# Performance work log

Measured on AMD Instinct MI355X. Metric: run time of the kernel, lower is better.

Reference implementation:

```python
import jax, jax.numpy as jnp
import numpy as np

_EPS = 1e-5

def _ln(x, g, b):
    m = jnp.mean(x, axis=-1, keepdims=True)
    v = jnp.var(x, axis=-1, keepdims=True)
    return (x - m) * jax.lax.rsqrt(v + _EPS) * g + b

def setup_inputs() -> dict:
    key = jax.random.key(0)
    ks = jax.random.split(key, 12)
    B, S, D = 8, 2048, 1024
    H = 2 * D          # hidden_dim = 2*n_embd
    A = H // 16        # adapt_dim = 128
    E = 8              # num_experts
    std = 1.0 / D ** 0.5
    astd = std * 0.01
    f = lambda k, shape, s: jax.random.normal(k, shape, dtype=jnp.float32) * s
    return {
        'x': f(ks[0], (B, S, D), 1.0),
        'expert_weights': f(ks[1], (B, S, E), 1.0),
        'w_up': f(ks[2], (H, D), std),
        'w_gate': f(ks[3], (H, D), std),
        'w_down': f(ks[4], (D, H), std),
        'w_pre': f(ks[5], (A, D), astd),
        'w_post': f(ks[6], (A, H), astd),
        'an_g': jnp.ones((A,), jnp.float32),
        'an_b': jnp.zeros((A,), jnp.float32),
        'w_aproj': f(ks[7], (H, A), astd),
        'w_exp': f(ks[8], (E, A, A), 0.01 / A ** 0.5),
        'eln_g': jnp.ones((E, A), jnp.float32),
        'eln_b': jnp.zeros((E, A), jnp.float32),
        'w_eproj': f(ks[9], (H, A), 0.01 / A ** 0.5),
        'w_out': f(ks[10], (D, H), 0.01 / A ** 0.5),
    }

def reference(x, expert_weights, w_up, w_gate, w_down, w_pre, w_post,
              an_g, an_b, w_aproj, w_exp, eln_g, eln_b, w_eproj, w_out):
    # ---- shared LLaDAExpert ----
    up = jnp.einsum('bsd,hd->bsh', x, w_up)
    gate = jnp.einsum('bsd,hd->bsh', x, w_gate)
    hidden = jax.nn.silu(gate) * up                      # [B,S,H]
    pre = jnp.einsum('bsd,ad->bsa', x, w_pre)            # pre_adapt(x), reused by experts
    adapt_in = _ln(pre, an_g, an_b)                      # [B,S,A]
    adapt_out = _ln(jnp.einsum('bsh,ah->bsa', hidden, w_post), an_g, an_b)
    aw = jax.nn.silu(jnp.clip(jnp.einsum('bsa,bta->bst', adapt_in, adapt_out), -5.0, 5.0))  # [B,S,S]
    adapt = jnp.einsum('bst,bta->bsa', aw, adapt_in)     # [B,S,A]
    hidden = hidden + 0.1 * jnp.einsum('bsa,ha->bsh', adapt, w_aproj)
    shared = jnp.einsum('bsh,dh->bsd', hidden, w_down)   # [B,S,D]
    combined = jnp.zeros_like(shared)
    E = w_exp.shape[0]
    for i in range(E):
        a = _ln(jnp.einsum('bsa,ca->bsc', pre, w_exp[i]), eln_g[i], eln_b[i])
        o = jnp.einsum('bsh,dh->bsd', jnp.einsum('bsc,hc->bsh', a, w_eproj), w_out)
        mask = expert_weights[:, :, i] > 0
        combined = jnp.where(mask[..., None], o, combined)
    return shared + 0.1 * combined
```

## Files before the change

### kernel.cpp

```cpp
#include <hip/hip_runtime.h>

#define TOK 16384
#define DD 1024
#define HH 2048
#define AA 128
#define EE 8
#define SS 2048
#define BB 8

typedef __attribute__((ext_vector_type(8))) short short8;
typedef __attribute__((ext_vector_type(4))) float floatx4;

__device__ __forceinline__ unsigned short f2b(float f) {
  unsigned u = __float_as_uint(f);
  u += 0x7fff + ((u >> 16) & 1);
  return (unsigned short)(u >> 16);
}
__device__ __forceinline__ float b2f(unsigned short h) {
  return __uint_as_float(((unsigned)h) << 16);
}

__device__ __forceinline__ void xcd_swizzle(int& bx, int& by) {
  const int nbx = gridDim.x, nby = gridDim.y;
  if ((nby & 7) == 0) {
    const int L = blockIdx.y * nbx + blockIdx.x;
    const int xcd = L & 7, idx = L >> 3;
    bx = idx % nbx;
    by = (xcd * (nby >> 3)) + idx / nbx;
  } else {
    bx = blockIdx.x; by = blockIdx.y;
  }
}

__device__ __forceinline__ void kloop_pipe(const short* Ap, int lda, const short* Bp, int ldb,
                                           short* As, short* Bs, int K,
                                           int tid, int q, int l15, int l7, int wm, int wn,
                                           floatx4 (*acc)[4])
{
  short8 pa[4], pb[4];
#pragma unroll
  for (int i = 0; i < 4; ++i) {
    pa[i] = *(const short8*)(Ap + (long)i*32*lda);
    pb[i] = *(const short8*)(Bp + (long)i*32*ldb);
  }
  for (int kt = 0; kt < K; kt += 64) {
#pragma unroll
    for (int i = 0; i < 4; ++i) {
      *(short8*)((char*)As + i*4096 + tid*16) = pa[i];
      *(short8*)((char*)Bs + i*4096 + tid*16) = pb[i];
    }
    __syncthreads();
    if (kt + 64 < K) {
#pragma unroll
      for (int i = 0; i < 4; ++i) {
        pa[i] = *(const short8*)(Ap + (long)i*32*lda + kt + 64);
        pb[i] = *(const short8*)(Bp + (long)i*32*ldb + kt + 64);
      }
    }
#pragma unroll
    for (int s = 0; s < 2; ++s) {
      short8 af[4], bf[4];
      const int slotoff = ((s*4 + q) ^ l7) * 16;
#pragma unroll
      for (int i = 0; i < 4; ++i) {
        af[i] = *(const short8*)((const char*)As + (wm*64 + i*16 + l15)*128 + slotoff);
        bf[i] = *(const short8*)((const char*)Bs + (wn*64 + i*16 + l15)*128 + slotoff);
      }
#pragma unroll
      for (int i = 0; i < 4; ++i)
#pragma unroll
        for (int j = 0; j < 4; ++j)
          acc[i][j] = __builtin_amdgcn_mfma_f32_16x16x32_bf16(af[i], bf[j], acc[i][j], 0, 0, 0);
    }
    __syncthreads();
  }
}

__global__ void cast_f32_bf16(const float* __restrict__ in, unsigned short* __restrict__ out, long n4) {
  long i = (long)blockIdx.x * blockDim.x + threadIdx.x;
  const long stride = (long)gridDim.x * blockDim.x;
  for (; i < n4; i += stride) {
    float4 v = ((const float4*)in)[i];
    ushort4 o;
    o.x = f2b(v.x); o.y = f2b(v.y); o.z = f2b(v.z); o.w = f2b(v.w);
    ((ushort4*)out)[i] = o;
  }
}

__global__ void transpose_cast(const float* __restrict__ in, unsigned short* __restrict__ out,
                               int R, int C) {
  __shared__ float t[32][33];
  const int lx = threadIdx.x & 31, ly = threadIdx.x >> 5;
  const int r0 = blockIdx.y * 32, c0 = blockIdx.x * 32;
#pragma unroll
  for (int i = 0; i < 32; i += 8)
    t[ly + i][lx] = in[(long)(r0 + ly + i) * C + (c0 + lx)];
  __syncthreads();
#pragma unroll
  for (int i = 0; i < 32; i += 8)
    out[(long)(c0 + ly + i) * R + (r0 + lx)] = f2b(t[lx][ly + i]);
}

template<int EPI>
__global__ __launch_bounds__(256)
void gemm_bt(const unsigned short* __restrict__ Ag, long sAz, int lda,
             const unsigned short* __restrict__ Bg, long sBz, int ldb,
             void* __restrict__ Cg, long sCz, int ldc,
             const unsigned short* __restrict__ Xg, long sXz, int ldx,
             int K)
{
  __shared__ __align__(16) short As[128*64];
  __shared__ __align__(16) short Bs[128*64];
  int bx, by; xcd_swizzle(bx, by);
  const int tid  = threadIdx.x;
  const int lane = tid & 63, wave = tid >> 6;
  const int q = lane >> 4, l15 = lane & 15, l7 = lane & 7;
  const int wm = wave & 1, wn = wave >> 1;

  const int arow = tid >> 3;
  const int kc8  = ((tid & 7) ^ (arow & 7)) * 8;

  const short* Ap = (const short*)Ag + (long)blockIdx.z*sAz + (long)(by*128 + arow)*lda + kc8;
  const short* Bp = (const short*)Bg + (long)blockIdx.z*sBz + (long)(bx*128 + arow)*ldb + kc8;

  floatx4 acc[4][4] = {};
  kloop_pipe(Ap, lda, Bp, ldb, As, Bs, K, tid, q, l15, l7, wm, wn, acc);

  const long cz = (long)blockIdx.z * sCz;
  const long xz = (long)blockIdx.z * sXz;
#pragma unroll
  for (int i = 0; i < 4; ++i)
#pragma unroll
    for (int j = 0; j < 4; ++j)
#pragma unroll
      for (int r = 0; r < 4; ++r) {
        const int row = by*128 + wm*64 + i*16 + q*4 + r;
        const int col = bx*128 + wn*64 + j*16 + l15;
        const long ci = cz + (long)row*ldc + col;
        float v = acc[i][j][r];
        if (EPI == 0) {
          ((float*)Cg)[ci] = v;
        } else if (EPI == 1) {
          v = v / (1.f + __expf(-v));
          ((unsigned short*)Cg)[ci] = f2b(v);
        } else if (EPI == 2) {
          float g = b2f(Xg[xz + (long)row*ldx + col]);
          ((unsigned short*)Cg)[ci] = f2b(v * g);
        } else if (EPI == 3) {
          ((unsigned short*)Cg)[ci] = f2b(v);
        } else if (EPI == 4) {
          v = fminf(fmaxf(v, -5.f), 5.f);
          v = v / (1.f + __expf(-v));
          ((unsigned short*)Cg)[ci] = f2b(v);
        } else if (EPI == 6) {
          ((unsigned short*)Cg)[ci] = f2b(0.1f * v);
        }
      }
}

__global__ __launch_bounds__(256)
void gemm_final(const unsigned short* __restrict__ hidp,
                const unsigned short* __restrict__ wdbp,
                const unsigned short* __restrict__ Fcp,
                const unsigned short* __restrict__ Wcp,
                float* __restrict__ outp)
{
  __shared__ __align__(16) short As[128*64];
  __shared__ __align__(16) short Bs[128*64];
  int bx, by; xcd_swizzle(bx, by);
  const int tid  = threadIdx.x;
  const int lane = tid & 63, wave = tid >> 6;
  const int q = lane >> 4, l15 = lane & 15, l7 = lane & 7;
  const int wm = wave & 1, wn = wave >> 1;
  const int arow = tid >> 3;
  const int kc8  = ((tid & 7) ^ (arow & 7)) * 8;

  floatx4 acc[4][4] = {};

  kloop_pipe((const short*)hidp + (long)(by*128 + arow)*HH + kc8, HH,
             (const short*)wdbp + (long)(bx*128 + arow)*HH + kc8, HH,
             As, Bs, HH, tid, q, l15, l7, wm, wn, acc);
  kloop_pipe((const short*)Fcp + (long)(by*128 + arow)*256 + kc8, 256,
             (const short*)Wcp + (long)(bx*128 + arow)*256 + kc8, 256,
             As, Bs, 256, tid, q, l15, l7, wm, wn, acc);

#pragma unroll
  for (int i = 0; i < 4; ++i)
#pragma unroll
    for (int j = 0; j < 4; ++j)
#pragma unroll
      for (int r = 0; r < 4; ++r) {
        const int row = by*128 + wm*64 + i*16 + q*4 + r;
        const int col = bx*128 + wn*64 + j*16 + l15;
        outp[(long)row*DD + col] = acc[i][j][r];
      }
}

__global__ void ln_rows(const float* __restrict__ X, const float* __restrict__ g,
                        const float* __restrict__ b, unsigned short* __restrict__ lnout,
                        unsigned short* __restrict__ rawout, unsigned short* __restrict__ tout)
{
  const int lane = threadIdx.x & 63, wave = threadIdx.x >> 6;
  const long t = (long)blockIdx.x*4 + wave;
  const float* x = X + t*AA;
  float x0 = x[lane], x1 = x[lane + 64];
  float s = x0 + x1, s2 = x0*x0 + x1*x1;
#pragma unroll
  for (int m = 1; m < 64; m <<= 1) {
    s  += __shfl_xor(s, m, 64);
    s2 += __shfl_xor(s2, m, 64);
  }
  float mean = s * (1.f/AA);
  float inv  = rsqrtf(s2*(1.f/AA) - mean*mean + 1e-5f);
  float y0 = (x0 - mean)*inv*g[lane] + b[lane];
  float y1 = (x1 - mean)*inv*g[lane+64] + b[lane+64];
  lnout[t*AA + lane]      = f2b(y0);
  lnout[t*AA + lane + 64] = f2b(y1);
  if (rawout) { rawout[t*AA+lane] = f2b(x0); rawout[t*AA+lane+64] = f2b(x1); }
  if (tout) {
    const long bb = t >> 11, si = t & (SS-1);
    tout[bb*(long)AA*SS + (long)lane*SS + si]      = f2b(y0);
    tout[bb*(long)AA*SS + (long)(lane+64)*SS + si] = f2b(y1);
  }
}

__global__ void expert_select_ln(const float* __restrict__ ew, const unsigned short* __restrict__ eall,
                                 const float* __restrict__ eg, const float* __restrict__ ebias,
                                 unsigned short* __restrict__ Fc)
{
  const int lane = threadIdx.x & 63, wave = threadIdx.x >> 6;
  const long t = (long)blockIdx.x*4 + wave;
  const float* w = ew + t*EE;
  int ie = -1;
#pragma unroll
  for (int i = 0; i < EE; ++i) if (w[i] > 0.f) ie = i;
  unsigned short o0 = 0, o1 = 0;
  if (ie >= 0) {
    float x0 = b2f(eall[t*(EE*AA) + ie*AA + lane]);
    float x1 = b2f(eall[t*(EE*AA) + ie*AA + lane + 64]);
    float s = x0 + x1, s2 = x0*x0 + x1*x1;
#pragma unroll
    for (int m = 1; m < 64; m <<= 1) { s += __shfl_xor(s, m, 64); s2 += __shfl_xor(s2, m, 64); }
    float mean = s * (1.f/AA);
    float inv  = rsqrtf(s2*(1.f/AA) - mean*mean + 1e-5f);
    o0 = f2b((x0-mean)*inv*eg[ie*AA+lane]    + ebias[ie*AA+lane]);
    o1 = f2b((x1-mean)*inv*eg[ie*AA+lane+64] + ebias[ie*AA+lane+64]);
  }
  Fc[t*256 + lane]      = o0;
  Fc[t*256 + lane + 64] = o1;
}

extern "C" void kernel_launch(void* const* d_in, const int* in_sizes, int n_in,
                              void* d_out, int out_size, void* d_ws, size_t ws_size,
                              hipStream_t stream)
{
  const float* x       = (const float*)d_in[0];
  const float* ew      = (const float*)d_in[1];
  const float* w_up    = (const float*)d_in[2];
  const float* w_gate  = (const float*)d_in[3];
  const float* w_down  = (const float*)d_in[4];
  const float* w_pre   = (const float*)d_in[5];
  const float* w_post  = (const float*)d_in[6];
  const float* an_g    = (const float*)d_in[7];
  const float* an_b    = (const float*)d_in[8];
  const float* w_aproj = (const float*)d_in[9];
  const float* w_exp   = (const float*)d_in[10];
  const float* eln_g   = (const float*)d_in[11];
  const float* eln_b   = (const float*)d_in[12];
  const float* w_eproj = (const float*)d_in[13];
  const float* w_out   = (const float*)d_in[14];

  char* ws = (char*)d_ws;
  size_t off = 0;
  auto take = [&](size_t bytes) { char* p = ws + off; off += (bytes + 255) & ~(size_t)255; return p; };

  unsigned short* Sc    = (unsigned short*)take((size_t)BB*SS*SS*2);
  unsigned short* xb    = Sc;
  unsigned short* eall  = (unsigned short*)((char*)Sc + (size_t)TOK*DD*2);
  unsigned short* hid   = (unsigned short*)take((size_t)TOK*HH*2);
  float*          pre   = (float*)take((size_t)TOK*AA*4);
  float*          postA = (float*)take((size_t)TOK*AA*4);
  unsigned short* Fc    = (unsigned short*)take((size_t)TOK*256*2);
  unsigned short* ain   = (unsigned short*)take((size_t)TOK*AA*2);
  unsigned short* ainT  = (unsigned short*)take((size_t)TOK*AA*2);
  unsigned short* aout  = (unsigned short*)take((size_t)TOK*AA*2);
  unsigned short* preb  = (unsigned short*)take((size_t)TOK*AA*2);
  unsigned short* wgb   = (unsigned short*)take((size_t)HH*DD*2);
  unsigned short* wub   = (unsigned short*)take((size_t)HH*DD*2);
  unsigned short* wdb   = (unsigned short*)take((size_t)DD*HH*2);
  unsigned short* wpostb= (unsigned short*)take((size_t)AA*HH*2);
  unsigned short* wpreb = (unsigned short*)take((size_t)AA*DD*2);
  unsigned short* wexpb = (unsigned short*)take((size_t)EE*AA*AA*2);
  unsigned short* Wc    = (unsigned short*)take((size_t)DD*256*2);
  (void)ws_size; (void)in_sizes; (void)n_in; (void)out_size;

  unsigned short* woutb  = hid;
  unsigned short* btT    = hid + (size_t)DD*HH;
  unsigned short* eprojT = btT;
  unsigned short* aprojT = btT + (size_t)AA*HH;

  cast_f32_bf16<<<1024, 256, 0, stream>>>(x,      xb,     (long)TOK*DD/4);
  cast_f32_bf16<<<256,  256, 0, stream>>>(w_gate, wgb,    (long)HH*DD/4);
  cast_f32_bf16<<<256,  256, 0, stream>>>(w_up,   wub,    (long)HH*DD/4);
  cast_f32_bf16<<<256,  256, 0, stream>>>(w_down, wdb,    (long)DD*HH/4);
  cast_f32_bf16<<<256,  256, 0, stream>>>(w_out,  woutb,  (long)DD*HH/4);
  cast_f32_bf16<<<64,   256, 0, stream>>>(w_post, wpostb, (long)AA*HH/4);
  cast_f32_bf16<<<32,   256, 0, stream>>>(w_pre,  wpreb,  (long)AA*DD/4);
  cast_f32_bf16<<<32,   256, 0, stream>>>(w_exp,  wexpb,  (long)EE*AA*AA/4);

  transpose_cast<<<dim3(AA/32, HH/32), 256, 0, stream>>>(w_eproj, eprojT, HH, AA);
  transpose_cast<<<dim3(AA/32, HH/32), 256, 0, stream>>>(w_aproj, aprojT, HH, AA);

  gemm_bt<6><<<dim3(1, DD/128, 2), 256, 0, stream>>>(
      woutb, (long)(wdb - woutb), HH,
      eprojT, (long)AA*HH, HH,
      Wc, AA, 256, nullptr, 0, 0, HH);

  gemm_bt<1><<<dim3(HH/128, TOK/128, 1), 256, 0, stream>>>(xb,0,DD, wgb,0,DD, hid,0,HH, nullptr,0,0, DD);
  gemm_bt<2><<<dim3(HH/128, TOK/128, 1), 256, 0, stream>>>(xb,0,DD, wub,0,DD, hid,0,HH, hid,0,HH, DD);

  gemm_bt<0><<<dim3(1, TOK/128, 1), 256, 0, stream>>>(xb,0,DD, wpreb,0,DD, pre,0,AA, nullptr,0,0, DD);
  ln_rows<<<TOK/4, 256, 0, stream>>>(pre, an_g, an_b, ain, preb, ainT);

  gemm_bt<3><<<dim3((EE*AA)/128, TOK/128, 1), 256, 0, stream>>>(preb,0,AA, wexpb,0,AA, eall,0,EE*AA, nullptr,0,0, AA);
  expert_select_ln<<<TOK/4, 256, 0, stream>>>(ew, eall, eln_g, eln_b, Fc);

  gemm_bt<0><<<dim3(1, TOK/128, 1), 256, 0, stream>>>(hid,0,HH, wpostb,0,HH, postA,0,AA, nullptr,0,0, HH);
  ln_rows<<<TOK/4, 256, 0, stream>>>(postA, an_g, an_b, aout, nullptr, nullptr);

  gemm_bt<4><<<dim3(SS/128, SS/128, BB), 256, 0, stream>>>(ain,(long)SS*AA,AA, aout,(long)SS*AA,AA,
                                                           Sc,(long)SS*SS,SS, nullptr,0,0, AA);
  gemm_bt<3><<<dim3(1, SS/128, BB), 256, 0, stream>>>(Sc,(long)SS*SS,SS, ainT,(long)AA*SS,SS,
                                                      Fc+AA,(long)SS*256,256, nullptr,0,0, SS);
  gemm_final<<<dim3(DD/128, TOK/128, 1), 256, 0, stream>>>(hid, wdb, Fc, Wc, (float*)d_out);
}
```

Measured before the change: 602.8 us.

## Add 256x256 tiled GEMM with direct-to-LDS loads for big GEMMs

```diff
diff --git a/kernel.cpp b/kernel.cpp
--- a/kernel.cpp
+++ b/kernel.cpp
@@ -30,6 +30,188 @@
   } else {
     bx = blockIdx.x; by = blockIdx.y;
   }
+}
+
+
+__device__ __forceinline__ void gload16(const short* g, short* l) {
+  __builtin_amdgcn_global_load_lds((__attribute__((address_space(1))) void*)(void*)g,
+                                   (__attribute__((address_space(3))) void*)l, 16, 0, 0);
+}
+
+__device__ __forceinline__ void stage_tile(const short* src, int ld, short* dst, int wave) {
+#pragma unroll
+  for (int i = 0; i < 4; ++i)
+    gload16(src + (long)i*64*ld, dst + i*4096 + wave*512);
+}
+
+__device__ __forceinline__ void ktile256(const char* Ab, const char* Bb,
+                                         short* Ad, short* Bd,
+                                         const short* nA, int nlda,
+                                         const short* nB, int nldb,
+                                         bool st, int wave,
+                                         int aOff, int bOff, int slot0, int slot1,
+                                         floatx4 (*acc)[4])
+{
+  short8 af[4][2], bf[4][2];
+#pragma unroll
+  for (int m = 0; m < 4; ++m) {
+    af[m][0] = *(const short8*)(Ab + aOff + m*2048 + slot0);
+    af[m][1] = *(const short8*)(Ab + aOff + m*2048 + slot1);
+  }
+#pragma unroll
+  for (int n = 0; n < 2; ++n) {
+    bf[n][0] = *(const short8*)(Bb + bOff + n*2048 + slot0);
+    bf[n][1] = *(const short8*)(Bb + bOff + n*2048 + slot1);
+  }
+  __builtin_amdgcn_s_barrier();
+  asm volatile("s_waitcnt lgkmcnt(0)" ::: "memory");
+  __builtin_amdgcn_s_setprio(1);
+#pragma unroll
+  for (int m = 0; m < 4; ++m)
+#pragma unroll
+    for (int n = 0; n < 2; ++n) {
+      acc[m][n] = __builtin_amdgcn_mfma_f32_16x16x32_bf16(af[m][0], bf[n][0], acc[m][n], 0, 0, 0);
+      acc[m][n] = __builtin_amdgcn_mfma_f32_16x16x32_bf16(af[m][1], bf[n][1], acc[m][n], 0, 0, 0);
+    }
+  __builtin_amdgcn_s_setprio(0);
+  __builtin_amdgcn_s_barrier();
+#pragma unroll
+  for (int n = 2; n < 4; ++n) {
+    bf[n][0] = *(const short8*)(Bb + bOff + n*2048 + slot0);
+    bf[n][1] = *(const short8*)(Bb + bOff + n*2048 + slot1);
+  }
+  __builtin_amdgcn_s_barrier();
+  asm volatile("s_waitcnt lgkmcnt(0)" ::: "memory");
+  __builtin_amdgcn_s_setprio(1);
+#pragma unroll
+  for (int m = 0; m < 4; ++m)
+#pragma unroll
+    for (int n = 2; n < 4; ++n) {
+      acc[m][n] = __builtin_amdgcn_mfma_f32_16x16x32_bf16(af[m][0], bf[n][0], acc[m][n], 0, 0, 0);
+      acc[m][n] = __builtin_amdgcn_mfma_f32_16x16x32_bf16(af[m][1], bf[n][1], acc[m][n], 0, 0, 0);
+    }
+  __builtin_amdgcn_s_setprio(0);
+  __builtin_amdgcn_s_barrier();
+#pragma unroll
+  for (int m = 0; m < 4; ++m) {
+    af[m][0] = *(const short8*)(Ab + aOff + (m+4)*2048 + slot0);
+    af[m][1] = *(const short8*)(Ab + aOff + (m+4)*2048 + slot1);
+  }
+  if (st) stage_tile(nB, nldb, Bd, wave);
+  __builtin_amdgcn_s_barrier();
+  asm volatile("s_waitcnt lgkmcnt(0)" ::: "memory");
+  __builtin_amdgcn_s_setprio(1);
+#pragma unroll
+  for (int m = 0; m < 4; ++m)
+#pragma unroll
+    for (int n = 0; n < 2; ++n) {
+      acc[m+4][n] = __builtin_amdgcn_mfma_f32_16x16x32_bf16(af[m][0], bf[n][0], acc[m+4][n], 0, 0, 0);
+      acc[m+4][n] = __builtin_amdgcn_mfma_f32_16x16x32_bf16(af[m][1], bf[n][1], acc[m+4][n], 0, 0, 0);
+    }
+  __builtin_amdgcn_s_setprio(0);
+  __builtin_amdgcn_s_barrier();
+  if (st) stage_tile(nA, nlda, Ad, wave);
+  __builtin_amdgcn_s_barrier();
+  __builtin_amdgcn_s_setprio(1);
+#pragma unroll
+  for (int m = 0; m < 4; ++m)
+#pragma unroll
+    for (int n = 2; n < 4; ++n) {
+      acc[m+4][n] = __builtin_amdgcn_mfma_f32_16x16x32_bf16(af[m][0], bf[n][0], acc[m+4][n], 0, 0, 0);
+      acc[m+4][n] = __builtin_amdgcn_mfma_f32_16x16x32_bf16(af[m][1], bf[n][1], acc[m+4][n], 0, 0, 0);
+    }
+  __builtin_amdgcn_s_setprio(0);
+  if (st) asm volatile("s_waitcnt vmcnt(8)" ::: "memory");
+  else    asm volatile("s_waitcnt vmcnt(0)" ::: "memory");
+  __builtin_amdgcn_s_barrier();
+}
+
+template<int EPI>
+__global__ __launch_bounds__(512, 2)
+void gemm256(const unsigned short* __restrict__ Ag, int lda,
+             const unsigned short* __restrict__ Bg, int ldb,
+             void* __restrict__ Cg, int ldc,
+             const unsigned short* __restrict__ Xg, int ldx,
+             int K1,
+             const unsigned short* __restrict__ A2g, int lda2,
+             const unsigned short* __restrict__ B2g, int ldb2,
+             int K2)
+{
+  __shared__ __align__(16) short As[2][256*64];
+  __shared__ __align__(16) short Bs[2][256*64];
+  int bx, by; xcd_swizzle(bx, by);
+  const int tid = threadIdx.x;
+  const int lane = tid & 63, wave = tid >> 6;
+  const int q = lane >> 4, l15 = lane & 15;
+  const int wm = wave >> 2, wn = wave & 3;
+
+  const int arow = tid >> 3;
+  const int kc8  = ((tid & 7) ^ (arow & 7)) * 8;
+
+  const short* a1 = (const short*)Ag + (long)(by*256 + arow)*lda + kc8;
+  const short* b1 = (const short*)Bg + (long)(bx*256 + arow)*ldb + kc8;
+  const short* a2 = A2g ? (const short*)A2g + (long)(by*256 + arow)*lda2 + kc8 : (const short*)0;
+  const short* b2 = B2g ? (const short*)B2g + (long)(bx*256 + arow)*ldb2 + kc8 : (const short*)0;
+  const int nt1 = K1 >> 6, nt = (K1 + K2) >> 6, niter = nt >> 1;
+
+  auto tA = [&](int T, const short*& p, int& ld) {
+    if (T < nt1) { p = a1 + T*64; ld = lda; } else { p = a2 + (T - nt1)*64; ld = lda2; }
+  };
+  auto tB = [&](int T, const short*& p, int& ld) {
+    if (T < nt1) { p = b1 + T*64; ld = ldb; } else { p = b2 + (T - nt1)*64; ld = ldb2; }
+  };
+
+  const int aOff  = (wm*128 + l15) * 128;
+  const int bOff  = (wn*64  + l15) * 128;
+  const int l7    = l15 & 7;
+  const int slot0 = ((0*4 + q) ^ l7) * 16;
+  const int slot1 = ((1*4 + q) ^ l7) * 16;
+
+  floatx4 acc[8][4] = {};
+
+  stage_tile(a1, lda, As[0], wave);
+  stage_tile(b1, ldb, Bs[0], wave);
+  {
+    const short *pa, *pb; int la, lb;
+    tA(1, pa, la); tB(1, pb, lb);
+    stage_tile(pa, la, As[1], wave);
+    stage_tile(pb, lb, Bs[1], wave);
+  }
+  asm volatile("s_waitcnt vmcnt(8)" ::: "memory");
+  __builtin_amdgcn_s_barrier();
+
+  for (int i = 0; i < niter; ++i) {
+    const int t2 = 2*i + 2;
+    const bool st = t2 < nt;
+    const short *na = a1, *nb = b1; int nla = lda, nlb = ldb;
+    if (st) { tA(t2, na, nla); tB(t2, nb, nlb); }
+    ktile256((const char*)As[0], (const char*)Bs[0], As[0], Bs[0],
+             na, nla, nb, nlb, st, wave, aOff, bOff, slot0, slot1, acc);
+    if (st) { tA(t2+1, na, nla); tB(t2+1, nb, nlb); }
+    ktile256((const char*)As[1], (const char*)Bs[1], As[1], Bs[1],
+             na, nla, nb, nlb, st, wave, aOff, bOff, slot0, slot1, acc);
+  }
+
+#pragma unroll
+  for (int m = 0; m < 8; ++m)
+#pragma unroll
+    for (int n = 0; n < 4; ++n)
+#pragma unroll
+      for (int r = 0; r < 4; ++r) {
+        const int row = by*256 + wm*128 + m*16 + q*4 + r;
+        const int col = bx*256 + wn*64  + n*16 + l15;
+        const long ci = (long)row*ldc + col;
+        float v = acc[m][n][r];
+        if (EPI == 0) {
+          ((float*)Cg)[ci] = v;
+        } else if (EPI == 1) {
+          v = v / (1.f + __expf(-v));
+          ((unsigned short*)Cg)[ci] = f2b(v);
+        } else if (EPI == 2) {
+          float g = b2f(Xg[(long)row*ldx + col]);
+          ((unsigned short*)Cg)[ci] = f2b(v * g);
+        }
+      }
 }
 
 __device__ __forceinline__ void kloop_pipe(const short* Ap, int lda, const short* Bp, int ldb,
@@ -158,44 +340,6 @@
       }
 }
 
-__global__ __launch_bounds__(256)
-void gemm_final(const unsigned short* __restrict__ hidp,
-                const unsigned short* __restrict__ wdbp,
-                const unsigned short* __restrict__ Fcp,
-                const unsigned short* __restrict__ Wcp,
-                float* __restrict__ outp)
-{
-  __shared__ __align__(16) short As[128*64];
-  __shared__ __align__(16) short Bs[128*64];
-  int bx, by; xcd_swizzle(bx, by);
-  const int tid  = threadIdx.x;
-  const int lane = tid & 63, wave = tid >> 6;
-  const int q = lane >> 4, l15 = lane & 15, l7 = lane & 7;
-  const int wm = wave & 1, wn = wave >> 1;
-  const int arow = tid >> 3;
-  const int kc8  = ((tid & 7) ^ (arow & 7)) * 8;
-
-  floatx4 acc[4][4] = {};
-
-  kloop_pipe((const short*)hidp + (long)(by*128 + arow)*HH + kc8, HH,
-             (const short*)wdbp + (long)(bx*128 + arow)*HH + kc8, HH,
-             As, Bs, HH, tid, q, l15, l7, wm, wn, acc);
-  kloop_pipe((const short*)Fcp + (long)(by*128 + arow)*256 + kc8, 256,
-             (const short*)Wcp + (long)(bx*128 + arow)*256 + kc8, 256,
-             As, Bs, 256, tid, q, l15, l7, wm, wn, acc);
-
-#pragma unroll
-  for (int i = 0; i < 4; ++i)
-#pragma unroll
-    for (int j = 0; j < 4; ++j)
-#pragma unroll
-      for (int r = 0; r < 4; ++r) {
-        const int row = by*128 + wm*64 + i*16 + q*4 + r;
-        const int col = bx*128 + wn*64 + j*16 + l15;
-        outp[(long)row*DD + col] = acc[i][j][r];
-      }
-}
-
 __global__ void ln_rows(const float* __restrict__ X, const float* __restrict__ g,
                         const float* __restrict__ b, unsigned short* __restrict__ lnout,
                         unsigned short* __restrict__ rawout, unsigned short* __restrict__ tout)
@@ -316,8 +460,10 @@
       eprojT, (long)AA*HH, HH,
       Wc, AA, 256, nullptr, 0, 0, HH);
 
-  gemm_bt<1><<<dim3(HH/128, TOK/128, 1), 256, 0, stream>>>(xb,0,DD, wgb,0,DD, hid,0,HH, nullptr,0,0, DD);
-  gemm_bt<2><<<dim3(HH/128, TOK/128, 1), 256, 0, stream>>>(xb,0,DD, wub,0,DD, hid,0,HH, hid,0,HH, DD);
+  gemm256<1><<<dim3(HH/256, TOK/256), 512, 0, stream>>>(
+      xb, DD, wgb, DD, hid, HH, nullptr, 0, DD, nullptr, 0, nullptr, 0, 0);
+  gemm256<2><<<dim3(HH/256, TOK/256), 512, 0, stream>>>(
+      xb, DD, wub, DD, hid, HH, hid, HH, DD, nullptr, 0, nullptr, 0, 0);
 
   gemm_bt<0><<<dim3(1, TOK/128, 1), 256, 0, stream>>>(xb,0,DD, wpreb,0,DD, pre,0,AA, nullptr,0,0, DD);
   ln_rows<<<TOK/4, 256, 0, stream>>>(pre, an_g, an_b, ain, preb, ainT);
@@ -332,5 +478,6 @@
                                                            Sc,(long)SS*SS,SS, nullptr,0,0, AA);
   gemm_bt<3><<<dim3(1, SS/128, BB), 256, 0, stream>>>(Sc,(long)SS*SS,SS, ainT,(long)AA*SS,SS,
                                                       Fc+AA,(long)SS*256,256, nullptr,0,0, SS);
-  gemm_final<<<dim3(DD/128, TOK/128, 1), 256, 0, stream>>>(hid, wdb, Fc, Wc, (float*)d_out);
-}
+  gemm256<0><<<dim3(DD/256, TOK/256), 512, 0, stream>>>(
+      hid, HH, wdb, HH, (float*)d_out, DD, nullptr, 0, HH, Fc, 256, Wc, 256, 256);
+}
```

New measurement: 587.4 us. 1.03x faster.
